# Kernel optimization log

Hardware: AMD Instinct MI355X
Metric: run time of the kernel (lower is better)

Reference implementation:

```python
import jax, jax.numpy as jnp
import numpy as np

K_HARRIS = 0.04

def _conv3x3(x, ker):
    # x: [B,1,H,W], ker: [1,1,3,3]; cross-correlation w/ padding 1 (matches torch F.conv2d)
    return jax.lax.conv_general_dilated(
        x, ker, window_strides=(1, 1), padding=((1, 1), (1, 1)),
        dimension_numbers=("NCHW", "OIHW", "NCHW"))


def setup_inputs() -> dict:
    key = jax.random.key(0)
    x = jax.random.normal(key, (16, 3, 1024, 1024), dtype=jnp.float32)
    return {"x": x, "k": 512, "patch_size": 5}


def reference(x, k, patch_size):
    B, C, H, W = x.shape
    dt = x.dtype
    margin = patch_size
    mask = jnp.zeros((H, W), dt).at[margin:H - margin, margin:W - margin].set(1.0)

    img = jnp.mean(x, axis=1, keepdims=True) if C != 1 else x  # [B,1,H,W]

    kx = jnp.array([[[[-1, 0, 1], [-1, 0, 1], [-1, 0, 1]]]], dt)
    ky = jnp.array([[[[-1, -1, -1], [0, 0, 0], [1, 1, 1]]]], dt)
    dx = _conv3x3(img, kx)
    dy = _conv3x3(img, ky)

    g = (jnp.array([[1, 2, 1], [2, 4, 2], [1, 2, 1]], dt) / 16.0)[None, None]
    Sxx = _conv3x3(dx * dx, g)
    Syy = _conv3x3(dy * dy, g)
    Sxy = _conv3x3(dx * dy, g)

    det = Sxx * Syy - Sxy ** 2
    trace = Sxx + Syy
    R = (det - K_HARRIS * trace ** 2).squeeze(1) * mask  # [B,H,W]

    _, idx = jax.lax.top_k(R.reshape(B, H * W), k)  # [B,k]
    coords = jnp.stack([idx // W, idx % W], axis=-1).astype(dt)  # [B,k,2] (row,col)
    coords = (coords / jnp.array([H, W], dt) - 0.5) * 2.0
    return jnp.clip(coords.reshape(B, k, 2), -1.0, 1.0)
```

## Files before the change

### kernel.cpp

```cpp
#include <hip/hip_runtime.h>
#include <stdint.h>

#define HH 1024
#define WW 1024
#define NB 16
#define KTOP 512
#define NBINS 4096
#define CAP 8192
#define ROWS 16

typedef unsigned long long u64;
typedef unsigned int u32;

__device__ __forceinline__ u32 fmap(float v) {
    u32 u = __float_as_uint(v);
    return (u & 0x80000000u) ? ~u : (u | 0x80000000u);
}
__device__ __forceinline__ float fadd(float a, float b){ return __fadd_rn(a,b); }
__device__ __forceinline__ float fsub(float a, float b){ return __fsub_rn(a,b); }
__device__ __forceinline__ float fmul(float a, float b){ return __fmul_rn(a,b); }
__device__ __forceinline__ float add3(float a, float b, float c){ return fadd(fadd(a,b),c); }
__device__ __forceinline__ float mean3(float a, float b, float c){
    return __fdiv_rn(add3(a,b,c), 3.0f);
}

__device__ __forceinline__ float g9(float w00,float w01,float w02,
                                    float w10,float w11,float w12,
                                    float w20,float w21,float w22){
    float s = fadd(w00, fmul(2.0f,w01));
    s = fadd(s, w02);
    s = fadd(s, fmul(2.0f,w10));
    s = fadd(s, fmul(4.0f,w11));
    s = fadd(s, fmul(2.0f,w12));
    s = fadd(s, w20);
    s = fadd(s, fmul(2.0f,w21));
    s = fadd(s, w22);
    return fmul(s, 0.0625f);
}
__device__ __forceinline__ u32 respkey(float Sxx,float Syy,float Sxy,bool masked){
    float det = fsub(fmul(Sxx,Syy), fmul(Sxy,Sxy));
    float tr  = fadd(Sxx,Syy);
    float R   = fsub(det, fmul(fmul(0.04f,tr),tr));
    if (masked) R = 0.0f;
    return fmap(R);
}

__device__ __forceinline__ float4 vmean(float4 a, float4 b, float4 c){
    return make_float4(mean3(a.x,b.x,c.x), mean3(a.y,b.y,c.y),
                       mean3(a.z,b.z,c.z), mean3(a.w,b.w,c.w));
}
__device__ __forceinline__ float4 vadd3(float4 a, float4 b, float4 c){
    return make_float4(add3(a.x,b.x,c.x), add3(a.y,b.y,c.y),
                       add3(a.z,b.z,c.z), add3(a.w,b.w,c.w));
}

__global__ __launch_bounds__(256, 2) void harris_a(const float* __restrict__ x,
                                                   u32* __restrict__ gmax) {
    const int b     = blockIdx.y;
    const int task  = blockIdx.x * 4 + (threadIdx.x >> 6);
    const int lane  = threadIdx.x & 63;
    const int strip = task & 3;
    const int y0    = (task >> 2) * ROWS;
    const int sx    = strip * 256;
    const int cx    = sx + 4 * lane;
    const int hx    = (lane < 32) ? max(sx - 4, 0) : min(sx + 256, WW - 4);
    const bool lo32 = (lane < 32);
    const float* p0 = x + (size_t)b * 3 * HH * WW;
    const float* p1 = p0 + HH * WW;
    const float* p2 = p1 + HH * WW;

    float4 z4 = make_float4(0.f,0.f,0.f,0.f);
    float4 m0=z4, m1=z4, m2=z4, h0=z4, h1=z4, h2=z4;
    float hma0=0.f,hma1=0.f,hma2=0.f, hmb0=0.f,hmb1=0.f,hmb2=0.f;
    float he0=0.f,he1=0.f,he2=0.f;
    float a1xx[4], a1yy[4], a1xy[4], a2xx[4], a2yy[4], a2xy[4];
    #pragma unroll
    for (int j = 0; j < 4; ++j) {
        a1xx[j]=0.f; a1yy[j]=0.f; a1xy[j]=0.f;
        a2xx[j]=0.f; a2yy[j]=0.f; a2xy[j]=0.f;
    }

    #pragma unroll
    for (int t = 0; t < ROWS + 4; ++t) {
        m0=m1; m1=m2; h0=h1; h1=h2;
        hma0=hma1; hma1=hma2; hmb0=hmb1; hmb1=hmb2;
        he0=he1; he1=he2;
        int ym = min(max(y0 - 2 + t, 0), HH - 1);
        size_t ro = (size_t)ym * WW;
        float4 a0 = *(const float4*)(p0 + ro + cx);
        float4 a1v = *(const float4*)(p1 + ro + cx);
        float4 a2v = *(const float4*)(p2 + ro + cx);
        m2 = vmean(a0, a1v, a2v);
        float4 b0 = *(const float4*)(p0 + ro + hx);
        float4 b1 = *(const float4*)(p1 + ro + hx);
        float4 b2 = *(const float4*)(p2 + ro + hx);
        {
            float ca0 = lo32 ? b0.z : b0.x, ca1 = lo32 ? b1.z : b1.x, ca2 = lo32 ? b2.z : b2.x;
            float cb0 = lo32 ? b0.w : b0.y, cb1 = lo32 ? b1.w : b1.y, cb2 = lo32 ? b2.w : b2.y;
            hma2 = mean3(ca0, ca1, ca2);
            hmb2 = mean3(cb0, cb1, cb2);
        }
        {
            float upw = __shfl_up(m2.w, 1);
            float dnx = __shfl_down(m2.x, 1);
            float lm  = (lane == 0)  ? hmb2 : upw;
            float rm  = (lane == 63) ? hma2 : dnx;
            h2 = make_float4(add3(lm,   m2.x, m2.y),
                             add3(m2.x, m2.y, m2.z),
                             add3(m2.y, m2.z, m2.w),
                             add3(m2.z, m2.w, rm));
            he2 = lo32 ? add3(hma2, hmb2, m2.x) : add3(m2.w, hma2, hmb2);
        }

        if (t >= 2) {
            float4 s = vadd3(m0, m1, m2);
            float sva = add3(hma0, hma1, hma2);
            float svb = add3(hmb0, hmb1, hmb2);
            float upsw = __shfl_up(s.w, 1);
            float dnsx = __shfl_down(s.x, 1);
            float sm1 = (lane == 0)  ? svb : upsw;
            float sp4 = (lane == 63) ? sva : dnsx;
            float dx0 = fsub(s.y, sm1);
            float dx1 = fsub(s.z, s.x);
            float dx2 = fsub(s.w, s.y);
            float dx3 = fsub(sp4, s.z);
            float updx = __shfl_up(dx3, 1);
            float dndx = __shfl_down(dx0, 1);
            float dxm1 = (lane == 0)  ? fsub(s.x, sva) : updx;
            float dxp4 = (lane == 63) ? fsub(svb, s.w) : dndx;
            float dy0 = fsub(h2.x, h0.x);
            float dy1 = fsub(h2.y, h0.y);
            float dy2 = fsub(h2.z, h0.z);
            float dy3 = fsub(h2.w, h0.w);
            float dye = fsub(he2, he0);
            float updy = __shfl_up(dy3, 1);
            float dndy = __shfl_down(dy0, 1);
            float dym1 = (lane == 0)  ? dye : updy;
            float dyp4 = (lane == 63) ? dye : dndy;
            float DX[6] = {dxm1, dx0, dx1, dx2, dx3, dxp4};
            float DY[6] = {dym1, dy0, dy1, dy2, dy3, dyp4};
            float pxx[6], pyy[6], pxy[6];
            #pragma unroll
            for (int i = 0; i < 6; ++i) {
                pxx[i] = fmul(DX[i], DX[i]);
                pyy[i] = fmul(DY[i], DY[i]);
                pxy[i] = fmul(DX[i], DY[i]);
            }

            if (t >= 4) {
                int y = y0 + t - 4;
                bool rowm = (y < 5) || (y > HH - 6);
                u32 k[4];
                #pragma unroll
                for (int j = 0; j < 4; ++j) {
                    float Sxx = fmul(fadd(fadd(fadd(a2xx[j], pxx[j]),
                                    fmul(2.0f,pxx[j+1])), pxx[j+2]), 0.0625f);
                    float Syy = fmul(fadd(fadd(fadd(a2yy[j], pyy[j]),
                                    fmul(2.0f,pyy[j+1])), pyy[j+2]), 0.0625f);
                    float Sxy = fmul(fadd(fadd(fadd(a2xy[j], pxy[j]),
                                    fmul(2.0f,pxy[j+1])), pxy[j+2]), 0.0625f);
                    int gx = cx + j;
                    bool mk = rowm || (gx < 5) || (gx > WW - 6);
                    k[j] = respkey(Sxx, Syy, Sxy, mk);
                }
                u32 km = max(max(k[0], k[1]), max(k[2], k[3]));
                #pragma unroll
                for (int off = 1; off < 16; off <<= 1)
                    km = max(km, (u32)__shfl_xor((int)km, off));
                if ((lane & 15) == 0)
                    gmax[((size_t)b << 14) | ((size_t)y << 4) | (u32)(strip * 4 + (lane >> 4))] = km;
            }
            #pragma unroll
            for (int j = 0; j < 4; ++j) {
                a2xx[j] = fadd(fadd(fadd(a1xx[j], fmul(2.0f,pxx[j])),
                               fmul(4.0f,pxx[j+1])), fmul(2.0f,pxx[j+2]));
                a2yy[j] = fadd(fadd(fadd(a1yy[j], fmul(2.0f,pyy[j])),
                               fmul(4.0f,pyy[j+1])), fmul(2.0f,pyy[j+2]));
                a2xy[j] = fadd(fadd(fadd(a1xy[j], fmul(2.0f,pxy[j])),
                               fmul(4.0f,pxy[j+1])), fmul(2.0f,pxy[j+2]));
                a1xx[j] = fadd(fadd(pxx[j], fmul(2.0f,pxx[j+1])), pxx[j+2]);
                a1yy[j] = fadd(fadd(pyy[j], fmul(2.0f,pyy[j+1])), pyy[j+2]);
                a1xy[j] = fadd(fadd(pxy[j], fmul(2.0f,pxy[j+1])), pxy[j+2]);
            }
        }
    }
}

__global__ __launch_bounds__(512) void select_b(const u32* __restrict__ gmax,
                                                u32* __restrict__ glist,
                                                u32* __restrict__ gcount,
                                                u32* __restrict__ cutb,
                                                u32* __restrict__ cnt) {
    __shared__ u32 hist[NBINS];
    __shared__ u32 wsum[8];
    __shared__ u32 s_cut, s_n;
    const int b = blockIdx.x;
    const int tid = threadIdx.x;
    const u32* gm = gmax + ((size_t)b << 14);
    u32 val[32];
    #pragma unroll
    for (int j = 0; j < 8; ++j) {
        uint4 v = ((const uint4*)gm)[tid + j * 512];
        val[j*4+0]=v.x; val[j*4+1]=v.y; val[j*4+2]=v.z; val[j*4+3]=v.w;
    }
    for (int i = tid; i < NBINS; i += 512) hist[i] = 0u;
    if (tid == 0) { s_n = 0u; cnt[b * 16] = 0u; }
    __syncthreads();
    #pragma unroll
    for (int j = 0; j < 32; ++j) atomicAdd(&hist[val[j] >> 20], 1u);
    __syncthreads();
    u32 lv[8], ls = 0;
    #pragma unroll
    for (int i = 0; i < 8; ++i) { lv[i] = hist[tid*8+i]; ls += lv[i]; }
    const int lane = tid & 63, w = tid >> 6;
    u32 v = ls;
    #pragma unroll
    for (int off = 1; off < 64; off <<= 1) {
        u32 t2 = (u32)__shfl_down((int)v, off);
        if (lane + off < 64) v += t2;
    }
    if (lane == 0) wsum[w] = v;
    __syncthreads();
    u32 excl = v - ls;
    #pragma unroll
    for (int i = 0; i < 8; ++i) if (i > w) excl += wsum[i];
    if (excl < KTOP && excl + ls >= KTOP) {
        u32 acc = excl;
        #pragma unroll
        for (int i = 7; i >= 0; --i) {
            acc += lv[i];
            if (acc >= KTOP) { s_cut = (u32)(tid*8 + i); break; }
        }
    }
    __syncthreads();
    const u32 cut = s_cut;
    u32* gl = glist + ((size_t)b << 14);
    #pragma unroll
    for (int j = 0; j < 8; ++j)
        #pragma unroll
        for (int kk = 0; kk < 4; ++kk) {
            u32 gv = val[j*4+kk];
            if ((gv >> 20) >= cut) {
                u32 q = atomicAdd(&s_n, 1u);
                gl[q] = (u32)(j*2048 + 4*tid + kk);
            }
        }
    __syncthreads();
    if (tid == 0) { gcount[b] = s_n; cutb[b] = cut; }
}

__device__ __forceinline__ u32 harris_px(const float* __restrict__ p0,
                                         const float* __restrict__ p1,
                                         const float* __restrict__ p2,
                                         int gy, int gx) {
    if (gy < 5 || gy > HH - 6 || gx < 5 || gx > WW - 6) return 0x80000000u;
    float m[5][5];
    #pragma unroll
    for (int r = 0; r < 5; ++r)
        #pragma unroll
        for (int c = 0; c < 5; ++c) {
            size_t o = (size_t)(gy - 2 + r) * WW + (gx - 2 + c);
            m[r][c] = mean3(p0[o], p1[o], p2[o]);
        }
    float pxx[3][3], pyy[3][3], pxy[3][3];
    #pragma unroll
    for (int pr = 0; pr < 3; ++pr) {
        float s[5], ht[3], hb[3];
        #pragma unroll
        for (int c = 0; c < 5; ++c) s[c] = add3(m[pr][c], m[pr+1][c], m[pr+2][c]);
        #pragma unroll
        for (int c = 0; c < 3; ++c) {
            ht[c] = add3(m[pr][c],   m[pr][c+1],   m[pr][c+2]);
            hb[c] = add3(m[pr+2][c], m[pr+2][c+1], m[pr+2][c+2]);
        }
        #pragma unroll
        for (int pc = 0; pc < 3; ++pc) {
            float dx = fsub(s[pc+2], s[pc]);
            float dy = fsub(hb[pc], ht[pc]);
            pxx[pr][pc] = fmul(dx, dx);
            pyy[pr][pc] = fmul(dy, dy);
            pxy[pr][pc] = fmul(dx, dy);
        }
    }
    float Sxx = g9(pxx[0][0],pxx[0][1],pxx[0][2],pxx[1][0],pxx[1][1],pxx[1][2],pxx[2][0],pxx[2][1],pxx[2][2]);
    float Syy = g9(pyy[0][0],pyy[0][1],pyy[0][2],pyy[1][0],pyy[1][1],pyy[1][2],pyy[2][0],pyy[2][1],pyy[2][2]);
    float Sxy = g9(pxy[0][0],pxy[0][1],pxy[0][2],pxy[1][0],pxy[1][1],pxy[1][2],pxy[2][0],pxy[2][1],pxy[2][2]);
    return respkey(Sxx, Syy, Sxy, false);
}

__global__ __launch_bounds__(256) void refine_c(const float* __restrict__ x,
                                                const u32* __restrict__ glist,
                                                const u32* __restrict__ gcount,
                                                const u32* __restrict__ cutb,
                                                u32* __restrict__ cnt,
                                                u64* __restrict__ cand) {
    __shared__ u64 sbuf[CAP];
    __shared__ u32 s_n, s_base;
    const int b = blockIdx.y;
    const u32 gc  = gcount[b];
    const u32 cut = cutb[b];
    const int tid = threadIdx.x;
    const int wv = tid >> 6, lane = tid & 63;
    if (tid == 0) s_n = 0u;
    __syncthreads();

    const u32 per = (gc + 31) >> 5;
    const u32 i0  = blockIdx.x * per;
    const u32 i1  = min(i0 + per, gc);
    const float* p0 = x + (size_t)b * 3 * HH * WW;
    const float* p1 = p0 + HH * WW;
    const float* p2 = p1 + HH * WW;
    const u32* gl = glist + ((size_t)b << 14);

    for (u32 i = i0 + wv; i < i1; i += 4) {
        u32 gid = gl[i];
        int gy = (int)(gid >> 4);
        int gx = (int)((gid & 15u) << 6) + lane;
        u32 key = harris_px(p0, p1, p2, gy, gx);
        bool pred = (key >> 20) >= cut;
        u64 mball = __ballot(pred);
        if (mball) {
            int first = __ffsll((unsigned long long)mball) - 1;
            u32 base = 0;
            if (lane == first) base = atomicAdd(&s_n, (u32)__popcll(mball));
            base = __shfl(base, first);
            if (pred) {
                u32 q = base + (u32)__popcll(mball & ((1ull << lane) - 1));
                if (q < CAP) sbuf[q] = ((u64)key << 32) | (u32)~((u32)(gy << 10) | (u32)gx);
            }
        }
    }
    __syncthreads();
    u32 n = min(s_n, (u32)CAP);
    if (tid == 0) s_base = atomicAdd(&cnt[b * 16], n);
    __syncthreads();
    u32 gb = s_base;
    u64* cb = cand + (size_t)b * CAP;
    for (u32 j = tid; j < n; j += 256) {
        u32 q = gb + j;
        if (q < CAP) cb[q] = sbuf[j];
    }
}

__global__ __launch_bounds__(1024) void sort_d(const u32* __restrict__ cnt,
                                               const u64* __restrict__ cand,
                                               float* __restrict__ out) {
    __shared__ u64 s[CAP];
    const int b = blockIdx.x;
    u32 n = cnt[b * 16];
    if (n > CAP) n = CAP;
    u32 P = 512;
    while (P < n) P <<= 1;
    for (u32 i = threadIdx.x; i < P; i += 1024)
        s[i] = (i < n) ? cand[(size_t)b * CAP + i] : 0ULL;
    __syncthreads();
    for (u32 size = 2; size <= P; size <<= 1) {
        for (u32 stride = size >> 1; stride > 0; stride >>= 1) {
            for (u32 t = threadIdx.x; t < (P >> 1); t += 1024) {
                u32 i = 2 * t - (t & (stride - 1));
                u32 j = i + stride;
                u64 a = s[i], c = s[j];
                bool desc = ((i & size) == 0);
                if (desc ? (a < c) : (a > c)) { s[i] = c; s[j] = a; }
            }
            __syncthreads();
        }
    }
    if (threadIdx.x < KTOP) {
        u64 k = s[threadIdx.x];
        u32 idx = ~(u32)k;
        u32 row = idx >> 10, col = idx & 1023;
        float rf = ((float)row * (1.0f / 1024.0f) - 0.5f) * 2.0f;
        float cf = ((float)col * (1.0f / 1024.0f) - 0.5f) * 2.0f;
        rf = fminf(fmaxf(rf, -1.0f), 1.0f);
        cf = fminf(fmaxf(cf, -1.0f), 1.0f);
        float* o = out + ((size_t)b * KTOP + threadIdx.x) * 2;
        o[0] = rf;
        o[1] = cf;
    }
}

extern "C" void kernel_launch(void* const* d_in, const int* in_sizes, int n_in,
                              void* d_out, int out_size, void* d_ws, size_t ws_size,
                              hipStream_t stream) {
    const float* x = (const float*)d_in[0];
    float* out = (float*)d_out;
    char* ws = (char*)d_ws;

    u32* gmax   = (u32*)ws;
    u32* glist  = (u32*)(ws + (1u << 20));
    u32* gcount = (u32*)(ws + (2u << 20));
    u32* cutb   = (u32*)(ws + (2u << 20) + 64);
    u32* cnt    = (u32*)(ws + (2u << 20) + 128);
    u64* cand   = (u64*)(ws + (2u << 20) + 2048);

    hipLaunchKernelGGL(harris_a, dim3(64, NB), dim3(256), 0, stream, x, gmax);
    hipLaunchKernelGGL(select_b, dim3(NB), dim3(512), 0, stream, gmax, glist, gcount, cutb, cnt);
    hipLaunchKernelGGL(refine_c, dim3(32, NB), dim3(256), 0, stream, x, glist, gcount, cutb, cnt, cand);
    hipLaunchKernelGGL(sort_d, dim3(NB), dim3(1024), 0, stream, cnt, cand, out);
}
```

Before: 102.6 us.

## Prefilter sort candidates by histogram cut, remap harris blocks per XCD, widen refine grid

The sort kernel now histograms the top 12 key bits of the candidates, finds the bin where the cumulative count reaches 512, and compacts only candidates at or above that bin before the bitonic sort. This shrinks the sort size. The harris block index is remapped so consecutive batches/rows land on the same XCD, aimed at L2 locality. The refine grid doubles to 64 blocks with a smaller shared buffer, raising parallelism but making overflow truncation more likely per block.

```diff
diff --git a/kernel.cpp b/kernel.cpp
--- a/kernel.cpp
+++ b/kernel.cpp
@@ -7,6 +7,8 @@
 #define KTOP 512
 #define NBINS 4096
 #define CAP 8192
+#define LCAP 4096
+#define RGRID 64
 #define ROWS 16
 
 typedef unsigned long long u64;
@@ -56,11 +58,15 @@
 
 __global__ __launch_bounds__(256, 2) void harris_a(const float* __restrict__ x,
                                                    u32* __restrict__ gmax) {
-    const int b     = blockIdx.y;
-    const int task  = blockIdx.x * 4 + (threadIdx.x >> 6);
+    const int lin   = blockIdx.y * 64 + blockIdx.x;
+    const int xcd   = lin & 7, ridx = lin >> 3;
+    const int nl    = xcd * 128 + ridx;
+    const int b     = nl >> 6;
+    const int chunk = nl & 63;
+    const int wid   = threadIdx.x >> 6;
     const int lane  = threadIdx.x & 63;
-    const int strip = task & 3;
-    const int y0    = (task >> 2) * ROWS;
+    const int strip = wid;
+    const int y0    = chunk * ROWS;
     const int sx    = strip * 256;
     const int cx    = sx + 4 * lane;
     const int hx    = (lane < 32) ? max(sx - 4, 0) : min(sx + 256, WW - 4);
@@ -294,7 +300,7 @@
                                                 const u32* __restrict__ cutb,
                                                 u32* __restrict__ cnt,
                                                 u64* __restrict__ cand) {
-    __shared__ u64 sbuf[CAP];
+    __shared__ u64 sbuf[LCAP];
     __shared__ u32 s_n, s_base;
     const int b = blockIdx.y;
     const u32 gc  = gcount[b];
@@ -304,7 +310,7 @@
     if (tid == 0) s_n = 0u;
     __syncthreads();
 
-    const u32 per = (gc + 31) >> 5;
+    const u32 per = (gc + RGRID - 1) / RGRID;
     const u32 i0  = blockIdx.x * per;
     const u32 i1  = min(i0 + per, gc);
     const float* p0 = x + (size_t)b * 3 * HH * WW;
@@ -326,12 +332,12 @@
             base = __shfl(base, first);
             if (pred) {
                 u32 q = base + (u32)__popcll(mball & ((1ull << lane) - 1));
-                if (q < CAP) sbuf[q] = ((u64)key << 32) | (u32)~((u32)(gy << 10) | (u32)gx);
-            }
-        }
-    }
-    __syncthreads();
-    u32 n = min(s_n, (u32)CAP);
+                if (q < LCAP) sbuf[q] = ((u64)key << 32) | (u32)~((u32)(gy << 10) | (u32)gx);
+            }
+        }
+    }
+    __syncthreads();
+    u32 n = min(s_n, (u32)LCAP);
     if (tid == 0) s_base = atomicAdd(&cnt[b * 16], n);
     __syncthreads();
     u32 gb = s_base;
@@ -346,17 +352,68 @@
                                                const u64* __restrict__ cand,
                                                float* __restrict__ out) {
     __shared__ u64 s[CAP];
+    __shared__ u32 wsum[16];
+    __shared__ u32 s_cut2, s_n2;
     const int b = blockIdx.x;
+    const int tid = threadIdx.x;
     u32 n = cnt[b * 16];
     if (n > CAP) n = CAP;
+    const u64* cb = cand + (size_t)b * CAP;
+
+    u32* hs = (u32*)s;
+    for (int i = tid; i < NBINS; i += 1024) hs[i] = 0u;
+    if (tid == 0) { s_n2 = 0u; s_cut2 = 0u; }
+    __syncthreads();
+    for (u32 i = tid; i < n; i += 1024)
+        atomicAdd(&hs[(u32)(cb[i] >> 52)], 1u);
+    __syncthreads();
+
+    {
+        u32 lv[4], ls = 0;
+        #pragma unroll
+        for (int i = 0; i < 4; ++i) { lv[i] = hs[tid*4 + i]; ls += lv[i]; }
+        const int lane = tid & 63, w = tid >> 6;
+        u32 v = ls;
+        #pragma unroll
+        for (int off = 1; off < 64; off <<= 1) {
+            u32 t2 = (u32)__shfl_down((int)v, off);
+            if (lane + off < 64) v += t2;
+        }
+        if (lane == 0) wsum[w] = v;
+        __syncthreads();
+        u32 excl = v - ls;
+        #pragma unroll
+        for (int i = 0; i < 16; ++i) if (i > w) excl += wsum[i];
+        if (excl < KTOP && excl + ls >= KTOP) {
+            u32 acc = excl;
+            #pragma unroll
+            for (int i = 3; i >= 0; --i) {
+                acc += lv[i];
+                if (acc >= KTOP) { s_cut2 = (u32)(tid*4 + i); break; }
+            }
+        }
+    }
+    __syncthreads();
+    const u32 c2 = s_cut2;
+    __syncthreads();
+
+    for (u32 i = tid; i < n; i += 1024) {
+        u64 k = cb[i];
+        if ((u32)(k >> 52) >= c2) {
+            u32 q = atomicAdd(&s_n2, 1u);
+            s[q] = k;
+        }
+    }
+    __syncthreads();
+    u32 n2 = s_n2;
     u32 P = 512;
-    while (P < n) P <<= 1;
-    for (u32 i = threadIdx.x; i < P; i += 1024)
-        s[i] = (i < n) ? cand[(size_t)b * CAP + i] : 0ULL;
-    __syncthreads();
+    while (P < n2) P <<= 1;
+    for (u32 i = n2 + tid; i < P; i += 1024) s[i] = 0ULL;
+    __syncthreads();
+
     for (u32 size = 2; size <= P; size <<= 1) {
         for (u32 stride = size >> 1; stride > 0; stride >>= 1) {
-            for (u32 t = threadIdx.x; t < (P >> 1); t += 1024) {
+            for (u32 t = tid; t < (P >> 1); t += 1024) {
                 u32 i = 2 * t - (t & (stride - 1));
                 u32 j = i + stride;
                 u64 a = s[i], c = s[j];
@@ -366,15 +423,15 @@
             __syncthreads();
         }
     }
-    if (threadIdx.x < KTOP) {
-        u64 k = s[threadIdx.x];
+    if (tid < KTOP) {
+        u64 k = s[tid];
         u32 idx = ~(u32)k;
         u32 row = idx >> 10, col = idx & 1023;
         float rf = ((float)row * (1.0f / 1024.0f) - 0.5f) * 2.0f;
         float cf = ((float)col * (1.0f / 1024.0f) - 0.5f) * 2.0f;
         rf = fminf(fmaxf(rf, -1.0f), 1.0f);
         cf = fminf(fmaxf(cf, -1.0f), 1.0f);
-        float* o = out + ((size_t)b * KTOP + threadIdx.x) * 2;
+        float* o = out + ((size_t)b * KTOP + tid) * 2;
         o[0] = rf;
         o[1] = cf;
     }
@@ -396,6 +453,6 @@
 
     hipLaunchKernelGGL(harris_a, dim3(64, NB), dim3(256), 0, stream, x, gmax);
     hipLaunchKernelGGL(select_b, dim3(NB), dim3(512), 0, stream, gmax, glist, gcount, cutb, cnt);
-    hipLaunchKernelGGL(refine_c, dim3(32, NB), dim3(256), 0, stream, x, glist, gcount, cutb, cnt, cand);
+    hipLaunchKernelGGL(refine_c, dim3(RGRID, NB), dim3(256), 0, stream, x, glist, gcount, cutb, cnt, cand);
     hipLaunchKernelGGL(sort_d, dim3(NB), dim3(1024), 0, stream, cnt, cand, out);
 }
```

After: 102.2 us (median of 2 runs). Within noise of the previous version (-0.4%).
